# Performance work log

Measured on AMD Instinct MI355X. Metric: run time of the kernel, lower is better.

Reference implementation:

```python
import jax, jax.numpy as jnp
import numpy as np

N, C, K2 = 40000, 128, 9  # active voxels, channels, 3x3 kernel taps
HEAD_OUT = {"hm": 3, "center": 2, "center_z": 1, "dim": 3, "rot": 2}
EPS = 1e-5
INIT_BIAS = -2.66


def setup_inputs() -> dict:
    key = jax.random.key(0)
    ks = jax.random.split(key, 16)
    feats = jax.random.normal(ks[0], (N, C), dtype=jnp.float32)
    # precomputed submanifold-conv neighbor indices (one per kernel tap, all valid)
    nbr_idx = jax.random.randint(ks[1], (N, K2), 0, N, dtype=jnp.int32)
    H = len(HEAD_OUT)
    inp = {"feats": feats, "nbr_idx": nbr_idx}
    # stacked 3x3 SubMConv weights for all heads (kaiming-ish scale)
    inp["W1"] = jax.random.normal(ks[2], (H, K2, C, C), dtype=jnp.float32) * (2.0 / (K2 * C)) ** 0.5
    inp["gamma"] = jnp.ones((H, C), jnp.float32)
    inp["beta"] = jnp.zeros((H, C), jnp.float32)
    for i, (name, oc) in enumerate(HEAD_OUT.items()):
        inp[f"w_{name}"] = jax.random.normal(ks[3 + i], (C, oc), dtype=jnp.float32) * (2.0 / C) ** 0.5
        inp[f"b_{name}"] = (jnp.full((oc,), INIT_BIAS, jnp.float32) if name == "hm"
                             else jnp.zeros((oc,), jnp.float32))
    return inp


def reference(feats, nbr_idx, W1, gamma, beta,
              w_hm, b_hm, w_center, b_center, w_center_z, b_center_z,
              w_dim, b_dim, w_rot, b_rot):
    # SubMConv2d as gather + contraction over kernel taps (shared by all heads)
    gathered = feats[nbr_idx]                       # [N, K2, C]
    y = jnp.einsum('nkc,hkcd->hnd', gathered, W1)   # [H, N, C]
    # BatchNorm1d (training-mode forward: biased batch stats over voxels) + ReLU
    mean = y.mean(axis=1, keepdims=True)
    var = y.var(axis=1, keepdims=True)
    y = jax.nn.relu((y - mean) * jax.lax.rsqrt(var + EPS) * gamma[:, None, :] + beta[:, None, :])
    # per-head 1x1 SubMConv with bias
    heads = [(w_hm, b_hm), (w_center, b_center), (w_center_z, b_center_z),
             (w_dim, b_dim), (w_rot, b_rot)]
    outs = [y[i] @ w + b for i, (w, b) in enumerate(heads)]
    # concat head outputs along channel: [N, 3+2+1+3+2] = [N, 11]
    return jnp.concatenate(outs, axis=-1)
```

## Files before the change

### kernel.cpp

```cpp
#include <hip/hip_runtime.h>
#include <stdint.h>

#define NVOX 40000
#define CCH  128
#define K2   9
#define NH   5
#define TILES 313

typedef __attribute__((ext_vector_type(8))) short bf16x8;
typedef __attribute__((ext_vector_type(4))) float f32x4;

__device__ __forceinline__ unsigned short f2b(float f) {
  union { float f; unsigned int u; } v; v.f = f;
  return (unsigned short)((v.u + 0x7fffu + ((v.u >> 16) & 1u)) >> 16);
}
__device__ __forceinline__ float b2f(unsigned short u) {
  union { unsigned int u; float f; } v; v.u = ((unsigned int)u) << 16;
  return v.f;
}
__device__ __forceinline__ void g2l16(const void* g, void* l) {
  __builtin_amdgcn_global_load_lds(
      (const __attribute__((address_space(1))) unsigned int*)g,
      (__attribute__((address_space(3))) unsigned int*)l, 16, 0, 0);
}
__device__ __forceinline__ int swz(int row, int col) {
  return row * 128 + ((((col >> 3) ^ (row & 15)) << 3) | (col & 7));
}

__global__ void prep(const float4* __restrict__ feats, ushort4* __restrict__ fb,
                     const float* __restrict__ w1, unsigned short* __restrict__ w1t) {
  __shared__ unsigned short t[128 * 34];
  int b = blockIdx.x;
  if (b < 5000) {
    int i = b * 256 + threadIdx.x;
    if (i < NVOX * CCH / 4) {
      float4 v = feats[i];
      ushort4 r;
      r.x = f2b(v.x); r.y = f2b(v.y); r.z = f2b(v.z); r.w = f2b(v.w);
      fb[i] = r;
    }
    return;
  }
  int bb = b - 5000;
  int tile = bb >> 2;
  int q = bb & 3;
  const float* src = w1 + (size_t)tile * 16384 + q * 32 * 128;
  for (int e = threadIdx.x; e < 4096; e += 256) {
    int c = e >> 7, d = e & 127;
    t[d * 34 + c] = f2b(src[e]);
  }
  __syncthreads();
  unsigned short* dst = w1t + (size_t)tile * 16384 + q * 32;
  for (int e = threadIdx.x; e < 4096; e += 256) {
    int d = e >> 5, c = e & 31;
    dst[d * 128 + c] = t[d * 34 + c];
  }
}

__device__ __forceinline__ void stageB(unsigned short* dstbuf, const unsigned short* wp,
                                       int wave, int lane) {
  int lcol = lane & 15, lrow = lane >> 4;
#pragma unroll
  for (int i = 0; i < 8; ++i) {
    int elem = wave * 4096 + i * 512;
    int row = (elem >> 7) + lrow;
    g2l16(wp + row * 128 + ((lcol ^ (row & 15)) << 3), &dstbuf[elem]);
  }
}

__global__ void __launch_bounds__(256, 2) conv_gemm(
    const unsigned short* __restrict__ fb,
    const int* __restrict__ nbr,
    const unsigned short* __restrict__ w1t,
    unsigned short* __restrict__ yb,
    float* __restrict__ sums)
{
  __shared__ unsigned short Bs[2][128 * 128];
  __shared__ int idxs[128 * K2];

  const int bid = blockIdx.x;
  const int s = bid / 40;
  const int r = bid % 40;
  const int h = r >> 3;
  const int x = r & 7;
  const int tile = s * 8 + x;
  if (tile >= TILES) return;
  const int n0 = tile * 128;

  const int tid = threadIdx.x;
  const int wave = tid >> 6;
  const int lane = tid & 63;
  const int m = lane & 15;
  const int quad = lane >> 4;
  const int wm = wave >> 1, wn = wave & 1;

  for (int i = tid; i < 128 * K2; i += 256) {
    int rr = i / K2;
    int kk = i - rr * K2;
    int gn = n0 + rr; if (gn > NVOX - 1) gn = NVOX - 1;
    idxs[i] = nbr[gn * K2 + kk];
  }

  stageB(Bs[0], w1t + (((size_t)h * K2 + 0) << 14), wave, lane);
  __syncthreads();

  f32x4 acc[4][4] = {};

  for (int k = 0; k < K2; ++k) {
    asm volatile("s_waitcnt vmcnt(0)" ::: "memory");
    __syncthreads();

    if (k + 1 < K2)
      stageB(Bs[(k + 1) & 1], w1t + (((size_t)h * K2 + k + 1) << 14), wave, lane);

    const unsigned short* Bcur = Bs[k & 1];

    const unsigned short* aptr[4];
#pragma unroll
    for (int mi = 0; mi < 4; ++mi) {
      int rowA = idxs[(wm * 64 + mi * 16 + m) * K2 + k];
      aptr[mi] = fb + (size_t)rowA * CCH + quad * 8;
    }

#pragma unroll
    for (int kc = 0; kc < 4; ++kc) {
      bf16x8 af[4], bfr[4];
#pragma unroll
      for (int mi = 0; mi < 4; ++mi)
        af[mi] = *(const bf16x8*)(aptr[mi] + kc * 32);
#pragma unroll
      for (int ni = 0; ni < 4; ++ni) {
        int row = wn * 64 + ni * 16 + m;
        bfr[ni] = *(const bf16x8*)&Bcur[row * CCH + (((kc * 4 + quad) ^ (row & 15)) << 3)];
      }
#pragma unroll
      for (int mi = 0; mi < 4; ++mi)
#pragma unroll
        for (int ni = 0; ni < 4; ++ni)
          acc[mi][ni] = __builtin_amdgcn_mfma_f32_16x16x32_bf16(af[mi], bfr[ni], acc[mi][ni], 0, 0, 0);
    }
  }

  unsigned short* epi = Bs[1];
#pragma unroll
  for (int mi = 0; mi < 4; ++mi)
#pragma unroll
    for (int ni = 0; ni < 4; ++ni)
#pragma unroll
      for (int rr = 0; rr < 4; ++rr) {
        int row = wm * 64 + mi * 16 + quad * 4 + rr;
        int col = wn * 64 + ni * 16 + m;
        epi[swz(row, col)] = f2b(acc[mi][ni][rr]);
      }
  __syncthreads();

  for (int i = tid; i < 2048; i += 256) {
    int row = i >> 4;
    int c = i & 15;
    if (n0 + row < NVOX)
      *(bf16x8*)(yb + ((size_t)h * NVOX + n0 + row) * CCH + c * 8) =
          *(const bf16x8*)&epi[row * 128 + ((c ^ (row & 15)) << 3)];
  }

  {
    int col = tid & 127, half = tid >> 7;
    int rbase = half * 64;
    int nvalid = NVOX - n0 - rbase;
    if (nvalid > 64) nvalid = 64;
    float sm = 0.f, q = 0.f;
    for (int rr = 0; rr < nvalid; ++rr) {
      float z = b2f(epi[swz(rbase + rr, col)]);
      sm += z; q += z * z;
    }
    if (nvalid > 0) {
      atomicAdd(&sums[h * CCH + col], sm);
      atomicAdd(&sums[NH * CCH + h * CCH + col], q);
    }
  }
}

__global__ void finalize_bn(const float* __restrict__ sums, const float* __restrict__ gamma,
                            const float* __restrict__ beta, float* __restrict__ ssb) {
  int h = blockIdx.x, c = threadIdx.x;
  float mean = sums[h * CCH + c] * (1.f / NVOX);
  float var = sums[NH * CCH + h * CCH + c] * (1.f / NVOX) - mean * mean;
  float rstd = rsqrtf(var + 1e-5f);
  float scale = rstd * gamma[h * CCH + c];
  ssb[h * CCH + c] = scale;
  ssb[NH * CCH + h * CCH + c] = beta[h * CCH + c] - mean * scale;
}

__global__ void __launch_bounds__(256) head_fuse(
    const unsigned short* __restrict__ yb, const float* __restrict__ ssb,
    const float* __restrict__ w_hm, const float* __restrict__ b_hm,
    const float* __restrict__ w_ce, const float* __restrict__ b_ce,
    const float* __restrict__ w_cz, const float* __restrict__ b_cz,
    const float* __restrict__ w_dm, const float* __restrict__ b_dm,
    const float* __restrict__ w_rt, const float* __restrict__ b_rt,
    float* __restrict__ out)
{
  __shared__ unsigned short t[64 * 128];
  __shared__ float pbuf[4][64][12];

  const int tid = threadIdx.x;
  const int v0 = blockIdx.x * 64;
  const int vx = tid & 63;
  const int qd = tid >> 6;

  float part[11];
#pragma unroll
  for (int j = 0; j < 11; ++j) part[j] = 0.f;

#pragma unroll
  for (int h = 0; h < NH; ++h) {
    __syncthreads();
#pragma unroll
    for (int i = 0; i < 4; ++i) {
      int idx = i * 256 + tid;
      int row = idx >> 4, c = idx & 15;
      *(bf16x8*)&t[row * 128 + ((c ^ (row & 15)) << 3)] =
          *(const bf16x8*)(yb + ((size_t)h * NVOX + v0 + row) * CCH + c * 8);
    }
    __syncthreads();

    const float* sc = ssb + h * CCH;
    const float* sh = ssb + NH * CCH + h * CCH;
    const float* wp; int oc, off;
    switch (h) {
      case 0: wp = w_hm; oc = 3; off = 0; break;
      case 1: wp = w_ce; oc = 2; off = 3; break;
      case 2: wp = w_cz; oc = 1; off = 5; break;
      case 3: wp = w_dm; oc = 3; off = 6; break;
      default: wp = w_rt; oc = 2; off = 9; break;
    }
#pragma unroll
    for (int qq = 0; qq < 4; ++qq) {
      int q8 = qd * 4 + qq;
      bf16x8 pk = *(const bf16x8*)&t[vx * 128 + ((q8 ^ (vx & 15)) << 3)];
#pragma unroll
      for (int e = 0; e < 8; ++e) {
        int d = q8 * 8 + e;
        float z = fmaf(b2f((unsigned short)pk[e]), sc[d], sh[d]);
        z = fmaxf(z, 0.f);
        const float* wr = wp + d * oc;
        part[off] = fmaf(z, wr[0], part[off]);
        if (oc > 1) part[off + 1] = fmaf(z, wr[1], part[off + 1]);
        if (oc > 2) part[off + 2] = fmaf(z, wr[2], part[off + 2]);
      }
    }
  }

#pragma unroll
  for (int j = 0; j < 11; ++j) pbuf[qd][vx][j] = part[j];
  __syncthreads();
  if (tid < 64) {
    float o[11];
#pragma unroll
    for (int j = 0; j < 11; ++j)
      o[j] = pbuf[0][tid][j] + pbuf[1][tid][j] + pbuf[2][tid][j] + pbuf[3][tid][j];
    o[0] += b_hm[0]; o[1] += b_hm[1]; o[2] += b_hm[2];
    o[3] += b_ce[0]; o[4] += b_ce[1];
    o[5] += b_cz[0];
    o[6] += b_dm[0]; o[7] += b_dm[1]; o[8] += b_dm[2];
    o[9] += b_rt[0]; o[10] += b_rt[1];
    float* op = out + (size_t)(v0 + tid) * 11;
#pragma unroll
    for (int j = 0; j < 11; ++j) op[j] = o[j];
  }
}

extern "C" void kernel_launch(void* const* d_in, const int* in_sizes, int n_in,
                              void* d_out, int out_size, void* d_ws, size_t ws_size,
                              hipStream_t stream) {
  const float* feats = (const float*)d_in[0];
  const int*   nbr   = (const int*)d_in[1];
  const float* W1    = (const float*)d_in[2];
  const float* gamma = (const float*)d_in[3];
  const float* beta  = (const float*)d_in[4];
  const float* w_hm = (const float*)d_in[5];  const float* b_hm = (const float*)d_in[6];
  const float* w_ce = (const float*)d_in[7];  const float* b_ce = (const float*)d_in[8];
  const float* w_cz = (const float*)d_in[9];  const float* b_cz = (const float*)d_in[10];
  const float* w_dm = (const float*)d_in[11]; const float* b_dm = (const float*)d_in[12];
  const float* w_rt = (const float*)d_in[13]; const float* b_rt = (const float*)d_in[14];
  float* out = (float*)d_out;

  char* ws = (char*)d_ws;
  unsigned short* w1t = (unsigned short*)ws;
  unsigned short* fb  = (unsigned short*)(ws + 11796480);
  unsigned short* yb  = (unsigned short*)(ws + 22036480);
  float* sums = (float*)(ws + 73236480);
  float* ssb  = (float*)(ws + 73241600);

  hipMemsetAsync(sums, 0, 2 * NH * CCH * sizeof(float), stream);
  prep<<<5180, 256, 0, stream>>>((const float4*)feats, (ushort4*)fb, W1, w1t);
  conv_gemm<<<1600, 256, 0, stream>>>(fb, nbr, w1t, yb, sums);
  finalize_bn<<<NH, CCH, 0, stream>>>(sums, gamma, beta, ssb);
  head_fuse<<<625, 256, 0, stream>>>(yb, ssb, w_hm, b_hm, w_ce, b_ce, w_cz, b_cz,
                                     w_dm, b_dm, w_rt, b_rt, out);
}
```

Baseline: 293.1 us.

## Stage gathered A rows into LDS with async double-buffering and compute BN stats from accumulators

The gathered feature rows for each kernel tap now go through LDS with async global-to-LDS loads. They are double-buffered alongside the weight tiles, so the next tap's A and B loads overlap the current tap's MFMAs, replacing direct global loads inside the inner loop. Per-column BN sum and sum-of-squares are now reduced from the fp32 accumulators through a small LDS partial table instead of a serial 64-row loop over bf16 values. The sums memset is folded into an extra prep block. LDS use doubles to about 128KB and launch bounds drop to one block per CU, which costs occupancy.

Result: faster. 277.7 us (-5.3%).

```diff
diff --git a/kernel.cpp b/kernel.cpp
--- a/kernel.cpp
+++ b/kernel.cpp
@@ -28,7 +28,8 @@
 }
 
 __global__ void prep(const float4* __restrict__ feats, ushort4* __restrict__ fb,
-                     const float* __restrict__ w1, unsigned short* __restrict__ w1t) {
+                     const float* __restrict__ w1, unsigned short* __restrict__ w1t,
+                     float* __restrict__ sums) {
   __shared__ unsigned short t[128 * 34];
   int b = blockIdx.x;
   if (b < 5000) {
@@ -41,6 +42,10 @@
     }
     return;
   }
+  if (b == 5180) {
+    for (int i = threadIdx.x; i < 2 * NH * CCH; i += 256) sums[i] = 0.f;
+    return;
+  }
   int bb = b - 5000;
   int tile = bb >> 2;
   int q = bb & 3;
@@ -68,14 +73,30 @@
   }
 }
 
-__global__ void __launch_bounds__(256, 2) conv_gemm(
+__device__ __forceinline__ void stageA(unsigned short* dstbuf, const unsigned short* fb,
+                                       const int* idxs, int k, int wave, int lane) {
+  int lcol = lane & 15, lrow = lane >> 4;
+  int ridx[8];
+#pragma unroll
+  for (int i = 0; i < 8; ++i)
+    ridx[i] = idxs[(wave * 32 + i * 4 + lrow) * K2 + k];
+#pragma unroll
+  for (int i = 0; i < 8; ++i) {
+    int row = wave * 32 + i * 4 + lrow;
+    g2l16(fb + (size_t)ridx[i] * CCH + ((lcol ^ (row & 15)) << 3),
+          &dstbuf[(wave * 32 + i * 4) * CCH]);
+  }
+}
+
+__global__ void __launch_bounds__(256, 1) conv_gemm(
     const unsigned short* __restrict__ fb,
     const int* __restrict__ nbr,
     const unsigned short* __restrict__ w1t,
     unsigned short* __restrict__ yb,
     float* __restrict__ sums)
 {
-  __shared__ unsigned short Bs[2][128 * 128];
+  __shared__ __align__(16) unsigned short Asb[2][128 * 128];
+  __shared__ __align__(16) unsigned short Bsb[2][128 * 128];
   __shared__ int idxs[128 * K2];
 
   const int bid = blockIdx.x;
@@ -90,48 +111,45 @@
   const int tid = threadIdx.x;
   const int wave = tid >> 6;
   const int lane = tid & 63;
-  const int m = lane & 15;
-  const int quad = lane >> 4;
+  const int lcol = lane & 15;
+  const int lrow = lane >> 4;
   const int wm = wave >> 1, wn = wave & 1;
+
+  stageB(Bsb[0], w1t + (((size_t)h * K2) << 14), wave, lane);
 
   for (int i = tid; i < 128 * K2; i += 256) {
     int rr = i / K2;
-    int kk = i - rr * K2;
     int gn = n0 + rr; if (gn > NVOX - 1) gn = NVOX - 1;
-    idxs[i] = nbr[gn * K2 + kk];
-  }
-
-  stageB(Bs[0], w1t + (((size_t)h * K2 + 0) << 14), wave, lane);
+    idxs[i] = nbr[gn * K2 + (i - rr * K2)];
+  }
+  __syncthreads();
+  stageA(Asb[0], fb, idxs, 0, wave, lane);
+  asm volatile("s_waitcnt vmcnt(0)" ::: "memory");
   __syncthreads();
 
   f32x4 acc[4][4] = {};
 
   for (int k = 0; k < K2; ++k) {
-    asm volatile("s_waitcnt vmcnt(0)" ::: "memory");
-    __syncthreads();
-
-    if (k + 1 < K2)
-      stageB(Bs[(k + 1) & 1], w1t + (((size_t)h * K2 + k + 1) << 14), wave, lane);
-
-    const unsigned short* Bcur = Bs[k & 1];
-
-    const unsigned short* aptr[4];
-#pragma unroll
-    for (int mi = 0; mi < 4; ++mi) {
-      int rowA = idxs[(wm * 64 + mi * 16 + m) * K2 + k];
-      aptr[mi] = fb + (size_t)rowA * CCH + quad * 8;
-    }
+    const int buf = k & 1;
+    if (k + 1 < K2) {
+      stageA(Asb[buf ^ 1], fb, idxs, k + 1, wave, lane);
+      stageB(Bsb[buf ^ 1], w1t + (((size_t)h * K2 + k + 1) << 14), wave, lane);
+    }
+    const unsigned short* Acur = Asb[buf];
+    const unsigned short* Bcur = Bsb[buf];
 
 #pragma unroll
     for (int kc = 0; kc < 4; ++kc) {
       bf16x8 af[4], bfr[4];
 #pragma unroll
-      for (int mi = 0; mi < 4; ++mi)
-        af[mi] = *(const bf16x8*)(aptr[mi] + kc * 32);
+      for (int mi = 0; mi < 4; ++mi) {
+        int row = wm * 64 + mi * 16 + lcol;
+        af[mi] = *(const bf16x8*)&Acur[row * CCH + (((kc * 4 + lrow) ^ (row & 15)) << 3)];
+      }
 #pragma unroll
       for (int ni = 0; ni < 4; ++ni) {
-        int row = wn * 64 + ni * 16 + m;
-        bfr[ni] = *(const bf16x8*)&Bcur[row * CCH + (((kc * 4 + quad) ^ (row & 15)) << 3)];
+        int row = wn * 64 + ni * 16 + lcol;
+        bfr[ni] = *(const bf16x8*)&Bcur[row * CCH + (((kc * 4 + lrow) ^ (row & 15)) << 3)];
       }
 #pragma unroll
       for (int mi = 0; mi < 4; ++mi)
@@ -139,19 +157,41 @@
         for (int ni = 0; ni < 4; ++ni)
           acc[mi][ni] = __builtin_amdgcn_mfma_f32_16x16x32_bf16(af[mi], bfr[ni], acc[mi][ni], 0, 0, 0);
     }
-  }
-
-  unsigned short* epi = Bs[1];
+
+    if (k + 1 < K2) {
+      asm volatile("s_waitcnt vmcnt(0)" ::: "memory");
+      __syncthreads();
+    }
+  }
+
+  const bool full = (n0 + 128 <= NVOX);
+
+  unsigned short* epi = Asb[1];
 #pragma unroll
   for (int mi = 0; mi < 4; ++mi)
 #pragma unroll
     for (int ni = 0; ni < 4; ++ni)
 #pragma unroll
       for (int rr = 0; rr < 4; ++rr) {
-        int row = wm * 64 + mi * 16 + quad * 4 + rr;
-        int col = wn * 64 + ni * 16 + m;
+        int row = wm * 64 + mi * 16 + lrow * 4 + rr;
+        int col = wn * 64 + ni * 16 + lcol;
         epi[swz(row, col)] = f2b(acc[mi][ni][rr]);
       }
+
+  float2* pb = (float2*)Bsb[1];
+#pragma unroll
+  for (int ni = 0; ni < 4; ++ni) {
+    float sm = 0.f, q = 0.f;
+#pragma unroll
+    for (int mi = 0; mi < 4; ++mi)
+#pragma unroll
+      for (int rr = 0; rr < 4; ++rr) {
+        float v = acc[mi][ni][rr];
+        if (!full && n0 + wm * 64 + mi * 16 + lrow * 4 + rr >= NVOX) v = 0.f;
+        sm += v; q += v * v;
+      }
+    pb[(wn * 64 + ni * 16 + lcol) * 9 + wm * 4 + lrow] = make_float2(sm, q);
+  }
   __syncthreads();
 
   for (int i = tid; i < 2048; i += 256) {
@@ -162,20 +202,15 @@
           *(const bf16x8*)&epi[row * 128 + ((c ^ (row & 15)) << 3)];
   }
 
-  {
-    int col = tid & 127, half = tid >> 7;
-    int rbase = half * 64;
-    int nvalid = NVOX - n0 - rbase;
-    if (nvalid > 64) nvalid = 64;
+  if (tid < 128) {
     float sm = 0.f, q = 0.f;
-    for (int rr = 0; rr < nvalid; ++rr) {
-      float z = b2f(epi[swz(rbase + rr, col)]);
-      sm += z; q += z * z;
-    }
-    if (nvalid > 0) {
-      atomicAdd(&sums[h * CCH + col], sm);
-      atomicAdd(&sums[NH * CCH + h * CCH + col], q);
-    }
+#pragma unroll
+    for (int c = 0; c < 8; ++c) {
+      float2 p = pb[tid * 9 + c];
+      sm += p.x; q += p.y;
+    }
+    atomicAdd(&sums[h * CCH + tid], sm);
+    atomicAdd(&sums[NH * CCH + h * CCH + tid], q);
   }
 }
 
@@ -291,8 +326,7 @@
   float* sums = (float*)(ws + 73236480);
   float* ssb  = (float*)(ws + 73241600);
 
-  hipMemsetAsync(sums, 0, 2 * NH * CCH * sizeof(float), stream);
-  prep<<<5180, 256, 0, stream>>>((const float4*)feats, (ushort4*)fb, W1, w1t);
+  prep<<<5181, 256, 0, stream>>>((const float4*)feats, (ushort4*)fb, W1, w1t, sums);
   conv_gemm<<<1600, 256, 0, stream>>>(fb, nbr, w1t, yb, sums);
   finalize_bn<<<NH, CCH, 0, stream>>>(sums, gamma, beta, ssb);
   head_fuse<<<625, 256, 0, stream>>>(yb, ssb, w_hm, b_hm, w_ce, b_ce, w_cz, b_cz,
```
